# Performance work log

Hardware: AMD Instinct MI355X
Metric: run time of the kernel (lower is better)

## Reference

```python
import jax, jax.numpy as jnp
import numpy as np

# Production-scale dims (see shape_source)
B, N_C, N_T = 2, 4096, 1024
D_X, D_S = 64, 3
K = 32                 # SGNP default k=32
RECALL = 0.95          # approx_min_k recall_target as in approx_knn
SX = SS = ST = 1.0     # scale_x_sim / scale_s_sim / scale_t_sim


def setup_inputs() -> dict:
    key = jax.random.key(0)
    ks = jax.random.split(key, 6)
    return {
        "x_ctx": jax.random.normal(ks[0], (B, N_C, D_X), jnp.float32),
        "s_ctx": jax.random.normal(ks[1], (B, N_C, D_S), jnp.float32),
        "t_ctx": jax.random.uniform(ks[2], (B, N_C, 1), dtype=jnp.float32),
        "mask_ctx": jnp.ones((B, N_C), dtype=bool),
        "x_test": jax.random.normal(ks[3], (B, N_T, D_X), jnp.float32),
        "s_test": jax.random.normal(ks[4], (B, N_T, D_S), jnp.float32),
        "t_test": jax.random.uniform(ks[5], (B, N_T, 1), dtype=jnp.float32),
    }


def _sq_cdist(q, r):
    # squared euclidean distance, [B,Nq,d] x [B,Nr,d] -> [B,Nq,Nr]
    qn = jnp.sum(q * q, axis=-1)
    rn = jnp.sum(r * r, axis=-1)
    return qn[:, :, None] + rn[:, None, :] - 2.0 * jnp.einsum("bqd,brd->bqr", q, r)


def _knn(qx, qs, qt, rx, rs, rt, mask):
    """Vectorized approx_knn: multi-modal distances, causal mask, top-k, gather."""
    inf = jnp.inf
    m = mask[:, None, :]                       # [B,1,Nr] -> masked refs get inf (as _safe_mask)
    d_x = jnp.where(m, _sq_cdist(qx, rx), inf)  # [B,Nq,Nr]
    d_s = jnp.where(m, _sq_cdist(qs, rs), inf)
    d_t = rt[:, None, :, 0] - qt[:, :, None, 0]  # signed time diff (r - q)
    d_t = jnp.where(m, d_t, inf)
    d_t = jnp.where(d_t <= 0, d_t, inf)          # causal_t mask
    d_sq = (SX * d_x) ** 2 + (SS * d_s) ** 2 + (ST * d_t) ** 2
    _, idx = jax.lax.approx_min_k(jax.lax.stop_gradient(d_sq), K, recall_target=RECALL)
    g = lambda d: jnp.take_along_axis(d, idx, axis=-1)  # [B,Nq,K]
    return idx, g(d_x), g(d_s), g(d_t)


def reference(x_ctx, s_ctx, t_ctx, mask_ctx, x_test, s_test, t_test):
    # ctx->ctx and test->ctx kNN (build_graph)
    idx_cc, dx_cc, ds_cc, dt_cc = _knn(x_ctx, s_ctx, t_ctx, x_ctx, s_ctx, t_ctx, mask_ctx)
    idx_ct, dx_ct, ds_ct, dt_ct = _knn(x_test, s_test, t_test, x_ctx, s_ctx, t_ctx, mask_ctx)

    # batch offsets into the flat node array [B*N_C ctx nodes, then B*N_T test nodes]
    off = jnp.arange(B) * N_C
    senders_cc = idx_cc.reshape(-1) + jnp.repeat(off, N_C * K)
    senders_ct = idx_ct.reshape(-1) + jnp.repeat(off, N_T * K)
    senders = jnp.concatenate([senders_cc, senders_ct])
    receivers = jnp.repeat(jnp.arange(B * (N_C + N_T)), K)

    cat = lambda a, b: jnp.concatenate([a.reshape(-1), b.reshape(-1)])
    d_x = cat(dx_cc, dx_ct)   # [B*(N_C+N_T)*K]
    d_s = cat(ds_cc, ds_ct)
    d_t = cat(dt_cc, dt_ct)
    edge_mask = jnp.isfinite(d_x) & jnp.isfinite(d_s) & jnp.isfinite(d_t)
    return senders, receivers, d_x, d_s, d_t, edge_mask
```

## Files before the change

### kernel.cpp

```cpp
#include <hip/hip_runtime.h>

namespace {
constexpr int kB  = 2;
constexpr int kNC = 4096;
constexpr int kNT = 1024;
constexpr int kDX = 64;
constexpr int kK  = 32;
constexpr int kNQ = kB * (kNC + kNT);
constexpr long long kE = (long long)kNQ * kK;
constexpr int QPW  = 4;
constexpr int WAVES = 4;
constexpr int QPB  = WAVES * QPW;
constexpr int TILE = 64;
constexpr int HALF = 2048;
constexpr int HT   = HALF / TILE;
constexpr float kBigFinite = 1e30f;
constexpr size_t kRNF     = 8192;
constexpr size_t kKeyOffB = kRNF * 4;
constexpr size_t kWsNeed  = kKeyOffB + (size_t)kNQ * 64 * 8;
}

__device__ __forceinline__ void resolve_q(int gid,
    const float* x_ctx, const float* s_ctx, const float* t_ctx,
    const float* x_test, const float* s_test, const float* t_test,
    int& b, const float*& qx, const float*& qs, const float*& qt)
{
    if (gid < kB * kNC) {
        b  = gid >> 12;
        qx = x_ctx + (size_t)gid * kDX;
        qs = s_ctx + (size_t)gid * 3;
        qt = t_ctx + gid;
    } else {
        const int g2 = gid - kB * kNC;
        b  = g2 >> 10;
        qx = x_test + (size_t)g2 * kDX;
        qs = s_test + (size_t)g2 * 3;
        qt = t_test + g2;
    }
}

__device__ __forceinline__ void insert_half(unsigned long long& listKey,
    unsigned long long keyQ, int lane, int base)
{
    const unsigned long long thr = __shfl(listKey, base + 31, 64);
    unsigned long long hb = __ballot(keyQ < thr);
    while (hb) {
        const int srcl = __ffsll((unsigned long long)hb) - 1;
        hb &= hb - 1;
        const unsigned long long K = __shfl(keyQ, srcl, 64);
        const unsigned long long lt = __ballot(listKey < K);
        const unsigned int half = base ? (unsigned int)(lt >> 32)
                                       : (unsigned int)lt;
        const int pos = __popc(half) + base;
        if (pos < base + 32) {
            const unsigned long long up = __shfl_up(listKey, 1, 64);
            if (lane >= base && lane < base + 32) {
                if (lane > pos)       listKey = up;
                else if (lane == pos) listKey = K;
            }
        }
    }
}

__global__ __launch_bounds__(256)
void prep_rn(const float* __restrict__ x, float* __restrict__ ws)
{
    const int r = blockIdx.x * 256 + threadIdx.x;
    const float4* xr = (const float4*)(x + (size_t)r * kDX);
    float rn = 0.f;
    #pragma unroll
    for (int j = 0; j < 16; ++j) {
        const float4 rv = xr[j];
        rn = fmaf(rv.x, rv.x, rn); rn = fmaf(rv.y, rv.y, rn);
        rn = fmaf(rv.z, rv.z, rn); rn = fmaf(rv.w, rv.w, rn);
    }
    ws[r] = rn;
}

__global__ __launch_bounds__(256, 4)
void knn_v6_part(const float* __restrict__ x_ctx, const float* __restrict__ s_ctx,
                 const float* __restrict__ t_ctx, const unsigned char* __restrict__ mask_ctx,
                 const float* __restrict__ x_test, const float* __restrict__ s_test,
                 const float* __restrict__ t_test, const float* __restrict__ rn_ws,
                 unsigned long long* __restrict__ keys)
{
    __shared__ float4 xt[2][TILE * 16];

    const int tid  = threadIdx.x;
    const int lane = tid & 63;
    const int w    = __builtin_amdgcn_readfirstlane(tid >> 6);
    const int blk  = blockIdx.x;
    const int g    = blk >> 1;
    const int h    = blk & 1;
    const int qbase = g * QPB;
    const int gid0  = qbase + w * QPW;

    int b;
    { int b_; const float *a, *c, *d;
      resolve_q(qbase, x_ctx, s_ctx, t_ctx, x_test, s_test, t_test, b_, a, c, d);
      b = b_; }

    const float4* xb4 = (const float4*)x_ctx + (size_t)b * kNC * (kDX / 4);
    const float*  rsp = s_ctx + (size_t)b * kNC * 3;
    const float*  rtp = t_ctx + (size_t)b * kNC;
    const float*  rnp = rn_ws + (size_t)b * kNC;
    const unsigned char* mp = mask_ctx + (size_t)b * kNC;

    const float* qxp[QPW];
    float qs0[QPW], qs1[QPW], qs2[QPW], qsn[QPW], qtv[QPW], qn[QPW];
    #pragma unroll
    for (int q = 0; q < QPW; ++q) {
        int bb; const float *qx, *qs, *qt;
        resolve_q(gid0 + q, x_ctx, s_ctx, t_ctx, x_test, s_test, t_test,
                  bb, qx, qs, qt);
        qxp[q] = qx;
        qs0[q] = qs[0]; qs1[q] = qs[1]; qs2[q] = qs[2]; qtv[q] = qt[0];
        qsn[q] = qs0[q]*qs0[q] + qs1[q]*qs1[q] + qs2[q]*qs2[q];
        const float ql = qx[lane];
        float s = ql * ql;
        #pragma unroll
        for (int off = 32; off > 0; off >>= 1) s += __shfl_xor(s, off, 64);
        qn[q] = s;
    }

    int sg[4], ss[4];
    #pragma unroll
    for (int i = 0; i < 4; ++i) {
        const int n = tid + 256 * i;
        const int r = n >> 4, j = n & 15;
        sg[i] = n;
        ss[i] = (r << 4) | (j ^ (r & 7));
    }
    const size_t hbase = (size_t)h * (HALF * 16);
    #pragma unroll
    for (int i = 0; i < 4; ++i) xt[0][ss[i]] = xb4[hbase + sg[i]];
    __syncthreads();

    const int lbase = lane << 4, lsw = lane & 7;
    const float INF = __builtin_inff();
    unsigned long long lst01 = ~0ull, lst23 = ~0ull;

    for (int t = 0; t < HT; ++t) {
        float4 p0, p1, p2, p3;
        const bool pre = (t + 1 < HT);
        if (pre) {
            const size_t nb = hbase + (size_t)(t + 1) * 1024;
            p0 = xb4[nb + sg[0]]; p1 = xb4[nb + sg[1]];
            p2 = xb4[nb + sg[2]]; p3 = xb4[nb + sg[3]];
        }
        const float4* buf = xt[t & 1];

        float dot[QPW] = {0.f, 0.f, 0.f, 0.f};
        #pragma unroll
        for (int j = 0; j < 16; ++j) {
            const float4 rv = buf[lbase | (j ^ lsw)];
            #pragma unroll
            for (int q = 0; q < QPW; ++q) {
                const float4 qv = ((const float4*)qxp[q])[j];
                dot[q] = fmaf(qv.x, rv.x, dot[q]);
                dot[q] = fmaf(qv.y, rv.y, dot[q]);
                dot[q] = fmaf(qv.z, rv.z, dot[q]);
                dot[q] = fmaf(qv.w, rv.w, dot[q]);
            }
        }

        const int r = h * HALF + t * TILE + lane;
        const float rn  = rnp[r];
        const float rs0 = rsp[r*3+0], rs1 = rsp[r*3+1], rs2 = rsp[r*3+2];
        const float rtv = rtp[r];
        const bool  m   = (mp[r] != 0);
        const float rsn = rs0*rs0 + rs1*rs1 + rs2*rs2;

        #pragma unroll
        for (int q = 0; q < QPW; ++q) {
            float d_x = qn[q] + rn - 2.0f * dot[q];
            const float sdot = qs0[q]*rs0 + qs1[q]*rs1 + qs2[q]*rs2;
            float d_s = qsn[q] + rsn - 2.0f * sdot;
            float d_t = rtv - qtv[q];
            if (!m) { d_x = INF; d_s = INF; d_t = INF; }
            if (!(d_t <= 0.f)) d_t = INF;
            const float v = d_x*d_x + d_s*d_s + d_t*d_t;
            const unsigned long long key =
                ((unsigned long long)__float_as_uint(v) << 32) | (unsigned)r;
            if (q < 2) insert_half(lst01, key, lane, (q & 1) * 32);
            else       insert_half(lst23, key, lane, (q & 1) * 32);
        }

        if (pre) {
            float4* nbuf = xt[(t + 1) & 1];
            nbuf[ss[0]] = p0; nbuf[ss[1]] = p1;
            nbuf[ss[2]] = p2; nbuf[ss[3]] = p3;
        }
        __syncthreads();
    }

    #pragma unroll
    for (int p = 0; p < 2; ++p) {
        const unsigned long long key = p ? lst23 : lst01;
        const int qidx = 2 * p + (lane >> 5);
        keys[((size_t)(gid0 + qidx) * 2 + h) * 32 + (lane & 31)] = key;
    }
}

__global__ __launch_bounds__(256)
void knn_v5_merge(const float* __restrict__ x_ctx, const float* __restrict__ s_ctx,
                  const float* __restrict__ t_ctx, const unsigned char* __restrict__ mask_ctx,
                  const float* __restrict__ x_test, const float* __restrict__ s_test,
                  const float* __restrict__ t_test,
                  const unsigned long long* __restrict__ keys,
                  float* __restrict__ out)
{
    __shared__ unsigned long long kbuf[WAVES][64];
    __shared__ unsigned long long merged[WAVES][32];

    const int tid  = threadIdx.x;
    const int lane = tid & 63;
    const int w    = tid >> 6;
    const int qid  = blockIdx.x * WAVES + w;

    int b; const float *qx, *qs, *qt;
    resolve_q(qid, x_ctx, s_ctx, t_ctx, x_test, s_test, t_test, b, qx, qs, qt);
    const float qs0_ = qs[0], qs1_ = qs[1], qs2_ = qs[2], qtv_ = qt[0];
    const float qsn_ = qs0_*qs0_ + qs1_*qs1_ + qs2_*qs2_;
    const float ql = qx[lane];
    float qn_ = ql * ql;
    #pragma unroll
    for (int off = 32; off > 0; off >>= 1) qn_ += __shfl_xor(qn_, off, 64);

    const unsigned long long mykey = keys[(size_t)qid * 64 + lane];
    kbuf[w][lane] = mykey;
    __syncthreads();

    int cnt = 0;
    const int ob = (lane < 32) ? 32 : 0;
    #pragma unroll
    for (int j = 0; j < 32; ++j) cnt += (kbuf[w][ob + j] < mykey) ? 1 : 0;
    const int pos = (lane & 31) + cnt;
    if (pos < 32) merged[w][pos] = mykey;
    __syncthreads();

    if (lane < kK) {
        const unsigned long long key = merged[w][lane];
        const int rsel = (int)(key & 0xFFFFFFFFull);

        const float*  rsp = s_ctx + (size_t)b * kNC * 3;
        const float*  rtp = t_ctx + (size_t)b * kNC;
        const unsigned char* mp = mask_ctx + (size_t)b * kNC;

        const float4* xr = (const float4*)(x_ctx + ((size_t)b * kNC + rsel) * kDX);
        const float4* qr = (const float4*)qx;
        float dot = 0.f, rn2 = 0.f;
        #pragma unroll
        for (int j = 0; j < 16; ++j) {
            const float4 rv = xr[j];
            const float4 qv = qr[j];
            rn2 = fmaf(rv.x, rv.x, rn2); rn2 = fmaf(rv.y, rv.y, rn2);
            rn2 = fmaf(rv.z, rv.z, rn2); rn2 = fmaf(rv.w, rv.w, rn2);
            dot = fmaf(qv.x, rv.x, dot); dot = fmaf(qv.y, rv.y, dot);
            dot = fmaf(qv.z, rv.z, dot); dot = fmaf(qv.w, rv.w, dot);
        }
        float d_x = qn_ + rn2 - 2.0f * dot;
        const float rs0 = rsp[rsel*3+0], rs1 = rsp[rsel*3+1], rs2 = rsp[rsel*3+2];
        const float rsn = rs0*rs0 + rs1*rs1 + rs2*rs2;
        const float sdot = qs0_*rs0 + qs1_*rs1 + qs2_*rs2;
        float d_s = qsn_ + rsn - 2.0f * sdot;
        const float dt_raw = rtp[rsel] - qtv_;
        const bool  m = (mp[rsel] != 0);
        const bool  causal = m && (dt_raw <= 0.f);

        const float em = causal ? 1.0f : 0.0f;
        const float d_x_out = m ? d_x : kBigFinite;
        const float d_s_out = m ? d_s : kBigFinite;
        const float d_t_out = causal ? dt_raw : kBigFinite;

        const size_t e = (size_t)qid * kK + (size_t)lane;
        out[e]                = (float)(rsel + b * kNC);
        out[(size_t)kE   + e] = (float)qid;
        out[(size_t)kE*2 + e] = d_x_out;
        out[(size_t)kE*3 + e] = d_s_out;
        out[(size_t)kE*4 + e] = d_t_out;
        out[(size_t)kE*5 + e] = em;
    }
}

__global__ __launch_bounds__(256, 4)
void knn_v4(const float* __restrict__ x_ctx, const float* __restrict__ s_ctx,
            const float* __restrict__ t_ctx, const unsigned char* __restrict__ mask_ctx,
            const float* __restrict__ x_test, const float* __restrict__ s_test,
            const float* __restrict__ t_test, float* __restrict__ out)
{
    __shared__ float4 xt[2][TILE * 16];
    const int tid  = threadIdx.x;
    const int lane = tid & 63;
    const int w    = __builtin_amdgcn_readfirstlane(tid >> 6);
    const int qbase = blockIdx.x * QPB;
    const int gid0  = qbase + w * QPW;
    int b;
    { int b_; const float *a, *c, *d;
      resolve_q(qbase, x_ctx, s_ctx, t_ctx, x_test, s_test, t_test, b_, a, c, d);
      b = b_; }
    const float4* xb4 = (const float4*)x_ctx + (size_t)b * kNC * (kDX / 4);
    const float*  rsp = s_ctx + (size_t)b * kNC * 3;
    const float*  rtp = t_ctx + (size_t)b * kNC;
    const unsigned char* mp = mask_ctx + (size_t)b * kNC;
    const float* qxp[QPW];
    float qs0[QPW], qs1[QPW], qs2[QPW], qsn[QPW], qtv[QPW], qn[QPW];
    #pragma unroll
    for (int q = 0; q < QPW; ++q) {
        int bb; const float *qx, *qs, *qt;
        resolve_q(gid0 + q, x_ctx, s_ctx, t_ctx, x_test, s_test, t_test, bb, qx, qs, qt);
        qxp[q] = qx;
        qs0[q] = qs[0]; qs1[q] = qs[1]; qs2[q] = qs[2]; qtv[q] = qt[0];
        qsn[q] = qs0[q]*qs0[q] + qs1[q]*qs1[q] + qs2[q]*qs2[q];
        const float ql = qx[lane];
        float s = ql * ql;
        #pragma unroll
        for (int off = 32; off > 0; off >>= 1) s += __shfl_xor(s, off, 64);
        qn[q] = s;
    }
    int sg[4], ss[4];
    #pragma unroll
    for (int i = 0; i < 4; ++i) {
        const int n = tid + 256 * i;
        const int r = n >> 4, j = n & 15;
        sg[i] = n; ss[i] = (r << 4) | (j ^ (r & 7));
    }
    #pragma unroll
    for (int i = 0; i < 4; ++i) xt[0][ss[i]] = xb4[sg[i]];
    __syncthreads();
    const int lbase = lane << 4, lsw = lane & 7;
    const float INF = __builtin_inff();
    unsigned long long lst01 = ~0ull, lst23 = ~0ull;
    for (int t = 0; t < kNC / TILE; ++t) {
        float4 p0, p1, p2, p3;
        const bool pre = (t + 1 < kNC / TILE);
        if (pre) {
            const size_t nb = (size_t)(t + 1) * 1024;
            p0 = xb4[nb + sg[0]]; p1 = xb4[nb + sg[1]];
            p2 = xb4[nb + sg[2]]; p3 = xb4[nb + sg[3]];
        }
        const float4* buf = xt[t & 1];
        float dot[QPW] = {0.f, 0.f, 0.f, 0.f};
        float rn = 0.f;
        #pragma unroll
        for (int j = 0; j < 16; ++j) {
            const float4 rv = buf[lbase | (j ^ lsw)];
            rn = fmaf(rv.x, rv.x, rn); rn = fmaf(rv.y, rv.y, rn);
            rn = fmaf(rv.z, rv.z, rn); rn = fmaf(rv.w, rv.w, rn);
            #pragma unroll
            for (int q = 0; q < QPW; ++q) {
                const float4 qv = ((const float4*)qxp[q])[j];
                dot[q] = fmaf(qv.x, rv.x, dot[q]);
                dot[q] = fmaf(qv.y, rv.y, dot[q]);
                dot[q] = fmaf(qv.z, rv.z, dot[q]);
                dot[q] = fmaf(qv.w, rv.w, dot[q]);
            }
        }
        const int r = t * TILE + lane;
        const float rs0 = rsp[r*3+0], rs1 = rsp[r*3+1], rs2 = rsp[r*3+2];
        const float rtv = rtp[r];
        const bool  m   = (mp[r] != 0);
        const float rsn = rs0*rs0 + rs1*rs1 + rs2*rs2;
        #pragma unroll
        for (int q = 0; q < QPW; ++q) {
            float d_x = qn[q] + rn - 2.0f * dot[q];
            const float sdot = qs0[q]*rs0 + qs1[q]*rs1 + qs2[q]*rs2;
            float d_s = qsn[q] + rsn - 2.0f * sdot;
            float d_t = rtv - qtv[q];
            if (!m) { d_x = INF; d_s = INF; d_t = INF; }
            if (!(d_t <= 0.f)) d_t = INF;
            const float v = d_x*d_x + d_s*d_s + d_t*d_t;
            const unsigned long long key =
                ((unsigned long long)__float_as_uint(v) << 32) | (unsigned)r;
            if (q < 2) insert_half(lst01, key, lane, (q & 1) * 32);
            else       insert_half(lst23, key, lane, (q & 1) * 32);
        }
        if (pre) {
            float4* nbuf = xt[(t + 1) & 1];
            nbuf[ss[0]] = p0; nbuf[ss[1]] = p1;
            nbuf[ss[2]] = p2; nbuf[ss[3]] = p3;
        }
        __syncthreads();
    }
    #pragma unroll
    for (int p = 0; p < 2; ++p) {
        const unsigned long long myl = p ? lst23 : lst01;
        const int qidx = 2 * p + (lane >> 5);
        const int rsel = (int)(myl & 0xFFFFFFFFull);
        const int gid  = gid0 + qidx;
        const float* qx  = (lane < 32) ? qxp[2*p] : qxp[2*p+1];
        const float qn_  = (lane < 32) ? qn [2*p] : qn [2*p+1];
        const float qs0_ = (lane < 32) ? qs0[2*p] : qs0[2*p+1];
        const float qs1_ = (lane < 32) ? qs1[2*p] : qs1[2*p+1];
        const float qs2_ = (lane < 32) ? qs2[2*p] : qs2[2*p+1];
        const float qsn_ = (lane < 32) ? qsn[2*p] : qsn[2*p+1];
        const float qtv_ = (lane < 32) ? qtv[2*p] : qtv[2*p+1];
        const float4* xr = (const float4*)(x_ctx + ((size_t)b * kNC + rsel) * kDX);
        const float4* qr = (const float4*)qx;
        float dot = 0.f, rn2 = 0.f;
        #pragma unroll
        for (int j = 0; j < 16; ++j) {
            const float4 rv = xr[j];
            const float4 qv = qr[j];
            rn2 = fmaf(rv.x, rv.x, rn2); rn2 = fmaf(rv.y, rv.y, rn2);
            rn2 = fmaf(rv.z, rv.z, rn2); rn2 = fmaf(rv.w, rv.w, rn2);
            dot = fmaf(qv.x, rv.x, dot); dot = fmaf(qv.y, rv.y, dot);
            dot = fmaf(qv.z, rv.z, dot); dot = fmaf(qv.w, rv.w, dot);
        }
        float d_x = qn_ + rn2 - 2.0f * dot;
        const float rs0 = rsp[rsel*3+0], rs1 = rsp[rsel*3+1], rs2 = rsp[rsel*3+2];
        const float rsn = rs0*rs0 + rs1*rs1 + rs2*rs2;
        const float sdot = qs0_*rs0 + qs1_*rs1 + qs2_*rs2;
        float d_s = qsn_ + rsn - 2.0f * sdot;
        const float dt_raw = rtp[rsel] - qtv_;
        const bool  m = (mp[rsel] != 0);
        const bool  causal = m && (dt_raw <= 0.f);
        const float em = causal ? 1.0f : 0.0f;
        const size_t e = (size_t)gid * kK + (size_t)(lane & 31);
        out[e]                = (float)(rsel + b * kNC);
        out[(size_t)kE   + e] = (float)gid;
        out[(size_t)kE*2 + e] = m ? d_x : kBigFinite;
        out[(size_t)kE*3 + e] = m ? d_s : kBigFinite;
        out[(size_t)kE*4 + e] = causal ? dt_raw : kBigFinite;
        out[(size_t)kE*5 + e] = em;
    }
}

extern "C" void kernel_launch(void* const* d_in, const int* in_sizes, int n_in,
                              void* d_out, int out_size, void* d_ws, size_t ws_size,
                              hipStream_t stream) {
    (void)in_sizes; (void)n_in; (void)out_size;
    const float* x_ctx = (const float*)d_in[0];
    const float* s_ctx = (const float*)d_in[1];
    const float* t_ctx = (const float*)d_in[2];
    const unsigned char* mask_ctx = (const unsigned char*)d_in[3];
    const float* x_test = (const float*)d_in[4];
    const float* s_test = (const float*)d_in[5];
    const float* t_test = (const float*)d_in[6];

    if (ws_size >= kWsNeed) {
        float* rn_ws = (float*)d_ws;
        unsigned long long* keys =
            (unsigned long long*)((char*)d_ws + kKeyOffB);
        prep_rn<<<dim3(32), dim3(256), 0, stream>>>(x_ctx, rn_ws);
        knn_v6_part<<<dim3(2 * kNQ / QPB), dim3(256), 0, stream>>>(
            x_ctx, s_ctx, t_ctx, mask_ctx, x_test, s_test, t_test, rn_ws, keys);
        knn_v5_merge<<<dim3(kNQ / WAVES), dim3(256), 0, stream>>>(
            x_ctx, s_ctx, t_ctx, mask_ctx, x_test, s_test, t_test, keys,
            (float*)d_out);
    } else {
        knn_v4<<<dim3(kNQ / QPB), dim3(256), 0, stream>>>(
            x_ctx, s_ctx, t_ctx, mask_ctx, x_test, s_test, t_test, (float*)d_out);
    }
}
```

Measured before the change: 371.0 us.

## Sort refs and queries by time bucket to skip causally masked reference tiles

Adds prep kernels that histogram, prefix-sum and scatter context references and queries into 256 time buckets per batch. Each block takes a group of time-sorted queries and scans only the permuted references whose bucket can be causal (time at or before the query's bucket). It falls back to scanning all references when fewer than K candidates exist. Blocks are launched in reverse order so the largest scans start first. This roughly halves the distance and top-k work, at the cost of several small extra launches, atomics, and indirect gathers of reference rows.

```diff
diff --git a/kernel.cpp b/kernel.cpp
--- a/kernel.cpp
+++ b/kernel.cpp
@@ -7,17 +7,30 @@
 constexpr int kDX = 64;
 constexpr int kK  = 32;
 constexpr int kNQ = kB * (kNC + kNT);
+constexpr int kQPB2 = kNC + kNT;
 constexpr long long kE = (long long)kNQ * kK;
 constexpr int QPW  = 4;
 constexpr int WAVES = 4;
 constexpr int QPB  = WAVES * QPW;
 constexpr int TILE = 64;
 constexpr int HALF = 2048;
-constexpr int HT   = HALF / TILE;
+constexpr int NGRP = kNQ / QPB;
+constexpr int GPB  = NGRP / kB;
 constexpr float kBigFinite = 1e30f;
-constexpr size_t kRNF     = 8192;
-constexpr size_t kKeyOffB = kRNF * 4;
-constexpr size_t kWsNeed  = kKeyOffB + (size_t)kNQ * 64 * 8;
+constexpr size_t kOffRn    = 0;
+constexpr size_t kOffPermR = 32768;
+constexpr size_t kOffPrefR = 65536;
+constexpr size_t kOffCntR  = 67840;
+constexpr size_t kOffPrefQ = 69888;
+constexpr size_t kOffCntQ  = 72192;
+constexpr size_t kOffQperm = 74240;
+constexpr size_t kOffKeys  = 115200;
+constexpr size_t kWsNeed   = kOffKeys + (size_t)kNQ * 64 * 8;
+}
+
+__device__ __forceinline__ int tbucket(float t) {
+    int b = (int)(t * 256.0f);
+    return b < 0 ? 0 : (b > 255 ? 255 : b);
 }
 
 __device__ __forceinline__ void resolve_q(int gid,
@@ -63,7 +76,7 @@
 }
 
 __global__ __launch_bounds__(256)
-void prep_rn(const float* __restrict__ x, float* __restrict__ ws)
+void prep_rn(const float* __restrict__ x, float* __restrict__ rn_ws)
 {
     const int r = blockIdx.x * 256 + threadIdx.x;
     const float4* xr = (const float4*)(x + (size_t)r * kDX);
@@ -74,44 +87,112 @@
         rn = fmaf(rv.x, rv.x, rn); rn = fmaf(rv.y, rv.y, rn);
         rn = fmaf(rv.z, rv.z, rn); rn = fmaf(rv.w, rv.w, rn);
     }
-    ws[r] = rn;
+    rn_ws[r] = rn;
+}
+
+__global__ __launch_bounds__(256)
+void prep_zero(int* __restrict__ cntR, int* __restrict__ cntQ)
+{
+    const int i = blockIdx.x * 256 + threadIdx.x;
+    if (i < 512) cntR[i] = 0;
+    else         cntQ[i - 512] = 0;
+}
+
+__global__ __launch_bounds__(256)
+void prep_hist(const float* __restrict__ t_ctx, const float* __restrict__ t_test,
+               int* __restrict__ cntR, int* __restrict__ cntQ)
+{
+    const int i = blockIdx.x * 256 + threadIdx.x;
+    if (i < 8192) {
+        const int b = i >> 12;
+        atomicAdd(&cntR[b * 256 + tbucket(t_ctx[i])], 1);
+    } else {
+        const int gid = i - 8192;
+        const int b = (gid < kB * kNC) ? (gid >> 12) : ((gid - kB * kNC) >> 10);
+        const float qt = (gid < kB * kNC) ? t_ctx[gid] : t_test[gid - kB * kNC];
+        atomicAdd(&cntQ[b * 256 + tbucket(qt)], 1);
+    }
+}
+
+__global__ __launch_bounds__(256)
+void prep_prefix(int* __restrict__ cntR, int* __restrict__ cntQ,
+                 int* __restrict__ prefR, int* __restrict__ prefQ)
+{
+    __shared__ int sh[256];
+    const int blk = blockIdx.x;
+    int* cnt  = (blk < 2) ? (cntR  + blk * 256) : (cntQ  + (blk - 2) * 256);
+    int* pref = (blk < 2) ? (prefR + blk * 257) : (prefQ + (blk - 2) * 257);
+    const int tid = threadIdx.x;
+    sh[tid] = cnt[tid];
+    __syncthreads();
+    if (tid == 0) {
+        int acc = 0;
+        for (int i = 0; i < 256; ++i) { const int v = sh[i]; sh[i] = acc; acc += v; }
+        pref[256] = acc;
+    }
+    __syncthreads();
+    pref[tid] = sh[tid];
+    cnt[tid]  = sh[tid];
+}
+
+__global__ __launch_bounds__(256)
+void prep_scatter(const float* __restrict__ t_ctx, const float* __restrict__ t_test,
+                  int* __restrict__ cntR, int* __restrict__ cntQ,
+                  int* __restrict__ permR, int* __restrict__ qperm)
+{
+    const int i = blockIdx.x * 256 + threadIdx.x;
+    if (i < 8192) {
+        const int b = i >> 12, rl = i & (kNC - 1);
+        const int pos = atomicAdd(&cntR[b * 256 + tbucket(t_ctx[i])], 1);
+        permR[b * kNC + pos] = rl;
+    } else {
+        const int gid = i - 8192;
+        const int b = (gid < kB * kNC) ? (gid >> 12) : ((gid - kB * kNC) >> 10);
+        const float qt = (gid < kB * kNC) ? t_ctx[gid] : t_test[gid - kB * kNC];
+        const int pos = atomicAdd(&cntQ[b * 256 + tbucket(qt)], 1);
+        qperm[b * kQPB2 + pos] = gid;
+    }
 }
 
 __global__ __launch_bounds__(256, 4)
-void knn_v6_part(const float* __restrict__ x_ctx, const float* __restrict__ s_ctx,
+void knn_v7_part(const float* __restrict__ x_ctx, const float* __restrict__ s_ctx,
                  const float* __restrict__ t_ctx, const unsigned char* __restrict__ mask_ctx,
                  const float* __restrict__ x_test, const float* __restrict__ s_test,
                  const float* __restrict__ t_test, const float* __restrict__ rn_ws,
-                 unsigned long long* __restrict__ keys)
+                 const int* __restrict__ permR, const int* __restrict__ prefR,
+                 const int* __restrict__ qperm, unsigned long long* __restrict__ keys)
 {
     __shared__ float4 xt[2][TILE * 16];
+    __shared__ int wred[WAVES];
 
     const int tid  = threadIdx.x;
     const int lane = tid & 63;
     const int w    = __builtin_amdgcn_readfirstlane(tid >> 6);
     const int blk  = blockIdx.x;
-    const int g    = blk >> 1;
+    const int gidx = (NGRP - 1) - (blk >> 1);
     const int h    = blk & 1;
-    const int qbase = g * QPB;
-    const int gid0  = qbase + w * QPW;
-
-    int b;
-    { int b_; const float *a, *c, *d;
-      resolve_q(qbase, x_ctx, s_ctx, t_ctx, x_test, s_test, t_test, b_, a, c, d);
-      b = b_; }
+    const int b    = (gidx >= GPB) ? 1 : 0;
+    const int gg   = gidx - b * GPB;
+
+    const int* qpm = qperm + b * kQPB2 + gg * QPB;
+    int gid_q[QPW];
+    #pragma unroll
+    for (int q = 0; q < QPW; ++q) gid_q[q] = qpm[w * QPW + q];
 
     const float4* xb4 = (const float4*)x_ctx + (size_t)b * kNC * (kDX / 4);
     const float*  rsp = s_ctx + (size_t)b * kNC * 3;
     const float*  rtp = t_ctx + (size_t)b * kNC;
     const float*  rnp = rn_ws + (size_t)b * kNC;
     const unsigned char* mp = mask_ctx + (size_t)b * kNC;
+    const int* pR = permR + b * kNC;
+    const int* pf = prefR + b * 257;
 
     const float* qxp[QPW];
     float qs0[QPW], qs1[QPW], qs2[QPW], qsn[QPW], qtv[QPW], qn[QPW];
     #pragma unroll
     for (int q = 0; q < QPW; ++q) {
         int bb; const float *qx, *qs, *qt;
-        resolve_q(gid0 + q, x_ctx, s_ctx, t_ctx, x_test, s_test, t_test,
+        resolve_q(gid_q[q], x_ctx, s_ctx, t_ctx, x_test, s_test, t_test,
                   bb, qx, qs, qt);
         qxp[q] = qx;
         qs0[q] = qs[0]; qs1[q] = qs[1]; qs2[q] = qs[2]; qtv[q] = qt[0];
@@ -123,33 +204,61 @@
         qn[q] = s;
     }
 
-    int sg[4], ss[4];
+    int vmax = 0;
+    #pragma unroll
+    for (int q = 0; q < QPW; ++q) {
+        const int qb = tbucket(qtv[q]);
+        int bound = pf[qb + 1];
+        if (pf[qb] < kK) bound = kNC;
+        vmax = bound > vmax ? bound : vmax;
+    }
+    if (lane == 0) wred[w] = vmax;
+    __syncthreads();
+    int bmax = wred[0];
+    #pragma unroll
+    for (int i = 1; i < WAVES; ++i) bmax = wred[i] > bmax ? wred[i] : bmax;
+
+    const int lo = h * HALF;
+    const int hi = bmax < lo + HALF ? bmax : lo + HALF;
+    const int ntile = (hi > lo) ? ((hi - lo + TILE - 1) >> 6) : 0;
+
+    int rrow[4], rcol[4], ssz[4];
     #pragma unroll
     for (int i = 0; i < 4; ++i) {
         const int n = tid + 256 * i;
-        const int r = n >> 4, j = n & 15;
-        sg[i] = n;
-        ss[i] = (r << 4) | (j ^ (r & 7));
-    }
-    const size_t hbase = (size_t)h * (HALF * 16);
-    #pragma unroll
-    for (int i = 0; i < 4; ++i) xt[0][ss[i]] = xb4[hbase + sg[i]];
+        rrow[i] = n >> 4; rcol[i] = n & 15;
+        ssz[i]  = (rrow[i] << 4) | (rcol[i] ^ (rrow[i] & 7));
+    }
+    if (ntile > 0) {
+        #pragma unroll
+        for (int i = 0; i < 4; ++i) {
+            const int o = pR[lo + rrow[i]];
+            xt[0][ssz[i]] = xb4[(size_t)o * 16 + rcol[i]];
+        }
+    }
     __syncthreads();
 
     const int lbase = lane << 4, lsw = lane & 7;
     const float INF = __builtin_inff();
     unsigned long long lst01 = ~0ull, lst23 = ~0ull;
 
-    for (int t = 0; t < HT; ++t) {
-        float4 p0, p1, p2, p3;
-        const bool pre = (t + 1 < HT);
+    for (int t = 0; t < ntile; ++t) {
+        const bool pre = (t + 1 < ntile);
+        float4 p4[4];
         if (pre) {
-            const size_t nb = hbase + (size_t)(t + 1) * 1024;
-            p0 = xb4[nb + sg[0]]; p1 = xb4[nb + sg[1]];
-            p2 = xb4[nb + sg[2]]; p3 = xb4[nb + sg[3]];
-        }
+            #pragma unroll
+            for (int i = 0; i < 4; ++i) {
+                const int o = pR[lo + (t + 1) * TILE + rrow[i]];
+                p4[i] = xb4[(size_t)o * 16 + rcol[i]];
+            }
+        }
+        const int o = pR[lo + t * TILE + lane];
+        const float rn  = rnp[o];
+        const float rs0 = rsp[o*3+0], rs1 = rsp[o*3+1], rs2 = rsp[o*3+2];
+        const float rtv = rtp[o];
+        const bool  m   = (mp[o] != 0);
+
         const float4* buf = xt[t & 1];
-
         float dot[QPW] = {0.f, 0.f, 0.f, 0.f};
         #pragma unroll
         for (int j = 0; j < 16; ++j) {
@@ -164,13 +273,7 @@
             }
         }
 
-        const int r = h * HALF + t * TILE + lane;
-        const float rn  = rnp[r];
-        const float rs0 = rsp[r*3+0], rs1 = rsp[r*3+1], rs2 = rsp[r*3+2];
-        const float rtv = rtp[r];
-        const bool  m   = (mp[r] != 0);
         const float rsn = rs0*rs0 + rs1*rs1 + rs2*rs2;
-
         #pragma unroll
         for (int q = 0; q < QPW; ++q) {
             float d_x = qn[q] + rn - 2.0f * dot[q];
@@ -181,15 +284,15 @@
             if (!(d_t <= 0.f)) d_t = INF;
             const float v = d_x*d_x + d_s*d_s + d_t*d_t;
             const unsigned long long key =
-                ((unsigned long long)__float_as_uint(v) << 32) | (unsigned)r;
+                ((unsigned long long)__float_as_uint(v) << 32) | (unsigned)o;
             if (q < 2) insert_half(lst01, key, lane, (q & 1) * 32);
             else       insert_half(lst23, key, lane, (q & 1) * 32);
         }
 
         if (pre) {
-            float4* nbuf = xt[(t + 1) & 1];
-            nbuf[ss[0]] = p0; nbuf[ss[1]] = p1;
-            nbuf[ss[2]] = p2; nbuf[ss[3]] = p3;
+            float4* nb = xt[(t + 1) & 1];
+            #pragma unroll
+            for (int i = 0; i < 4; ++i) nb[ssz[i]] = p4[i];
         }
         __syncthreads();
     }
@@ -197,8 +300,8 @@
     #pragma unroll
     for (int p = 0; p < 2; ++p) {
         const unsigned long long key = p ? lst23 : lst01;
-        const int qidx = 2 * p + (lane >> 5);
-        keys[((size_t)(gid0 + qidx) * 2 + h) * 32 + (lane & 31)] = key;
+        const int gsel = (lane < 32) ? gid_q[2*p] : gid_q[2*p+1];
+        keys[((size_t)gsel * 2 + h) * 32 + (lane & 31)] = key;
     }
 }
 
@@ -439,12 +542,25 @@
     const float* t_test = (const float*)d_in[6];
 
     if (ws_size >= kWsNeed) {
-        float* rn_ws = (float*)d_ws;
-        unsigned long long* keys =
-            (unsigned long long*)((char*)d_ws + kKeyOffB);
-        prep_rn<<<dim3(32), dim3(256), 0, stream>>>(x_ctx, rn_ws);
-        knn_v6_part<<<dim3(2 * kNQ / QPB), dim3(256), 0, stream>>>(
-            x_ctx, s_ctx, t_ctx, mask_ctx, x_test, s_test, t_test, rn_ws, keys);
+        char* ws = (char*)d_ws;
+        float* rn_ws = (float*)(ws + kOffRn);
+        int*   permR = (int*)(ws + kOffPermR);
+        int*   prefR = (int*)(ws + kOffPrefR);
+        int*   cntR  = (int*)(ws + kOffCntR);
+        int*   prefQ = (int*)(ws + kOffPrefQ);
+        int*   cntQ  = (int*)(ws + kOffCntQ);
+        int*   qperm = (int*)(ws + kOffQperm);
+        unsigned long long* keys = (unsigned long long*)(ws + kOffKeys);
+
+        prep_zero   <<<dim3(4),  dim3(256), 0, stream>>>(cntR, cntQ);
+        prep_rn     <<<dim3(32), dim3(256), 0, stream>>>(x_ctx, rn_ws);
+        prep_hist   <<<dim3(72), dim3(256), 0, stream>>>(t_ctx, t_test, cntR, cntQ);
+        prep_prefix <<<dim3(4),  dim3(256), 0, stream>>>(cntR, cntQ, prefR, prefQ);
+        prep_scatter<<<dim3(72), dim3(256), 0, stream>>>(t_ctx, t_test, cntR, cntQ,
+                                                         permR, qperm);
+        knn_v7_part <<<dim3(2 * NGRP), dim3(256), 0, stream>>>(
+            x_ctx, s_ctx, t_ctx, mask_ctx, x_test, s_test, t_test,
+            rn_ws, permR, prefR, qperm, keys);
         knn_v5_merge<<<dim3(kNQ / WAVES), dim3(256), 0, stream>>>(
             x_ctx, s_ctx, t_ctx, mask_ctx, x_test, s_test, t_test, keys,
             (float*)d_out);
```

After: 527.3 us. 1.42x slower.
